# Kernel optimization log

Hardware: AMD Instinct MI355X
Metric: run time of the kernel (lower is better)

The kernel has to match this reference:

```python
import jax, jax.numpy as jnp
import numpy as np

K = 3  # kernel_size

def _bn(x, g, b, m, v, eps=1e-5):
    # inference-mode BatchNorm2d over channel axis 1
    sh = (1, -1, 1, 1)
    return (x - m.reshape(sh)) * (g.reshape(sh) / jnp.sqrt(v.reshape(sh) + eps)) + b.reshape(sh)

def setup_inputs() -> dict:
    key = jax.random.key(0)
    ks = jax.random.split(key, 12)
    B, C, H, W, OC = 8, 128, 96, 96, 256
    k2 = K * K
    x = jax.random.normal(ks[0], (B, C, H, W), jnp.float32)
    # get_weight grouped 1x1 conv: [C*9,1,1,1] stored compactly as [C,9]
    w1 = jax.random.normal(ks[1], (C, k2), jnp.float32) * 0.1
    # generate_feature grouped 3x3 conv (groups=C, multiplier 9): OIHW [C*9,1,3,3]
    gf_w = jax.random.normal(ks[2], (C * k2, 1, K, K), jnp.float32) * 0.1
    bn1_g = jax.random.uniform(ks[3], (C * k2,), jnp.float32, 0.5, 1.5)
    bn1_b = jax.random.normal(ks[4], (C * k2,), jnp.float32) * 0.1
    bn1_m = jax.random.normal(ks[5], (C * k2,), jnp.float32) * 0.1
    bn1_v = jax.random.uniform(ks[6], (C * k2,), jnp.float32, 0.5, 1.5)
    conv_w = jax.random.normal(ks[7], (OC, C, K, K), jnp.float32) * (1.0 / np.sqrt(C * k2))
    conv_b = jax.random.normal(ks[8], (OC,), jnp.float32) * 0.1
    bn2_g = jax.random.uniform(ks[9], (OC,), jnp.float32, 0.5, 1.5)
    bn2_b = jax.random.normal(ks[10], (OC,), jnp.float32) * 0.1
    bn2_m = jax.random.normal(ks[11], (OC,), jnp.float32) * 0.1
    bn2_v = jax.random.uniform(jax.random.fold_in(key, 99), (OC,), jnp.float32, 0.5, 1.5)
    return {"x": x, "w1": w1, "gf_w": gf_w, "bn1_g": bn1_g, "bn1_b": bn1_b,
            "bn1_m": bn1_m, "bn1_v": bn1_v, "conv_w": conv_w, "conv_b": conv_b,
            "bn2_g": bn2_g, "bn2_b": bn2_b, "bn2_m": bn2_m, "bn2_v": bn2_v}

def reference(x, w1, gf_w, bn1_g, bn1_b, bn1_m, bn1_v, conv_w, conv_b, bn2_g, bn2_b, bn2_m, bn2_v):
    B, C, H, W = x.shape
    k2 = K * K
    # --- get_weight: AvgPool2d(k=3, pad=1, stride=1, count_include_pad) + grouped 1x1 conv ---
    pooled = jax.lax.reduce_window(x, 0.0, jax.lax.add, (1, 1, K, K), (1, 1, 1, 1),
                                   [(0, 0), (0, 0), (1, 1), (1, 1)]) / float(k2)
    weight = jnp.einsum('bchw,cn->bcnhw', pooled, w1)  # [B,C,9,H,W]
    attn = jax.nn.softmax(weight, axis=2)
    # --- generate_feature: depthwise 3x3 conv (groups=C, mult 9) + BN + ReLU ---
    feat = jax.lax.conv_general_dilated(x, gf_w, (1, 1), [(1, 1), (1, 1)],
                                        dimension_numbers=('NCHW', 'OIHW', 'NCHW'),
                                        feature_group_count=C)
    feat = jax.nn.relu(_bn(feat, bn1_g, bn1_b, bn1_m, bn1_v)).reshape(B, C, k2, H, W)
    # --- attention reweight + space-to-depth rearrange 'b c (n1 n2) h w -> b c (h n1) (w n2)' ---
    wd = (feat * attn).reshape(B, C, K, K, H, W)
    wd = wd.transpose(0, 1, 4, 2, 5, 3).reshape(B, C, H * K, W * K)
    # --- final conv k=3 stride=3 + BN + ReLU ---
    out = jax.lax.conv_general_dilated(wd, conv_w, (K, K), [(0, 0), (0, 0)],
                                       dimension_numbers=('NCHW', 'OIHW', 'NCHW'))
    out = out + conv_b.reshape(1, -1, 1, 1)
    return jax.nn.relu(_bn(out, bn2_g, bn2_b, bn2_m, bn2_v))
```

## Files before the change

kernel.cpp:

```cpp
#include <hip/hip_runtime.h>
#include <hip/hip_bf16.h>


#define CCH  128
#define OCN  256
#define HH   96
#define WWD  96
#define KCH  1152
#define PIMG 9216
#define BNP  64
#define NBLK 144
#define CC   32
#define KC   288
#define VP   296
#define NT   512

using short8   = __attribute__((ext_vector_type(8))) short;
using f32x4    = __attribute__((ext_vector_type(4))) float;
using f32x2    = __attribute__((ext_vector_type(2))) float;
using ushort2v = __attribute__((ext_vector_type(2))) ushort;

__device__ __forceinline__ ushort bf16bits(float f) {
    __hip_bfloat16 h = __float2bfloat16(f);
    return *reinterpret_cast<ushort*>(&h);
}

struct NB { f32x2 p[4]; float s; };

__global__ void prep_kernel(const float* __restrict__ W2, const float* __restrict__ gfw,
                            const float* __restrict__ bn1g, const float* __restrict__ bn1b,
                            const float* __restrict__ bn1m, const float* __restrict__ bn1v,
                            const float* __restrict__ w1,
                            ushort* __restrict__ W2bf, float* __restrict__ gws,
                            float* __restrict__ shiftv, float* __restrict__ w1s) {
    int i = blockIdx.x * 256 + threadIdx.x;
    if (i < OCN * KCH) {
        W2bf[i] = bf16bits(W2[i]);
    } else if (i < OCN * KCH + KCH) {
        const int ch = i - OCN * KCH;
        const float sc = bn1g[ch] * rsqrtf(bn1v[ch] + 1e-5f);
        shiftv[ch] = bn1b[ch] - bn1m[ch] * sc;
        #pragma unroll
        for (int t = 0; t < 9; ++t) gws[ch * 12 + t] = gfw[ch * 9 + t] * sc;
    } else if (i < OCN * KCH + KCH + CCH) {
        const int c = i - OCN * KCH - KCH;
        #pragma unroll
        for (int n = 0; n < 9; ++n)
            w1s[c * 12 + n] = w1[c * 9 + n] * (1.f / 9.f) * 1.4426950408889634f;
    }
}

template<bool FAST>
__global__ __launch_bounds__(NT, 4) void rfa_dp_kernel(
    const float* __restrict__ x,
    const float* __restrict__ w1,   const float* __restrict__ gfw,
    const float* __restrict__ bn1g, const float* __restrict__ bn1b,
    const float* __restrict__ bn1m, const float* __restrict__ bn1v,
    const float* __restrict__ W2f,
    const ushort* __restrict__ W2bf, const float* __restrict__ gws,
    const float* __restrict__ shiftv, const float* __restrict__ w1s,
    const float* __restrict__ cbias,
    const float* __restrict__ bn2g, const float* __restrict__ bn2b,
    const float* __restrict__ bn2m, const float* __restrict__ bn2v,
    float* __restrict__ out)
{
    __shared__ ushort vlds[2][BNP * VP];

    const int bid = blockIdx.x;
    const int wk  = (bid & 7) * NBLK + (bid >> 3);
    const int b   = wk / NBLK;
    const int P0  = (wk % NBLK) * BNP;

    const int tid  = threadIdx.x;
    const int lane = tid & 63;
    const int wid  = __builtin_amdgcn_readfirstlane(tid >> 6);

    const int px = lane;
    const int p  = P0 + px;
    const int h  = p / WWD;
    const int w  = p - h * WWD;
    const int l15 = lane & 15;
    const int lhi = lane >> 4;

    int off9[9];
    f32x2 okp[4];
    float ok8;
    {
        float okr[3], okc[3];
        int hro[3], wxc[3];
        #pragma unroll
        for (int d = 0; d < 3; ++d) {
            int hy = h + d - 1;
            okr[d] = ((unsigned)hy < (unsigned)HH) ? 1.f : 0.f;
            hro[d] = ((hy < 0) ? 0 : (hy > 95 ? 95 : hy)) * WWD;
            int wx = w + d - 1;
            okc[d] = ((unsigned)wx < (unsigned)WWD) ? 1.f : 0.f;
            wxc[d] = (wx < 0) ? 0 : (wx > 95 ? 95 : wx);
        }
        #pragma unroll
        for (int dy = 0; dy < 3; ++dy)
            #pragma unroll
            for (int dx = 0; dx < 3; ++dx) off9[dy*3+dx] = hro[dy] + wxc[dx];
        okp[0] = f32x2{okr[0]*okc[0], okr[0]*okc[1]};
        okp[1] = f32x2{okr[0]*okc[2], okr[1]*okc[0]};
        okp[2] = f32x2{okr[1]*okc[1], okr[1]*okc[2]};
        okp[3] = f32x2{okr[2]*okc[0], okr[2]*okc[1]};
        ok8    = okr[2]*okc[2];
    }

    f32x4 acc[2][4] = {};
    const float* xb = x + (size_t)b * CCH * PIMG;
    const int abase = (wid * 32 + l15) * KCH + lhi * 8;

    auto chan = [&](int q) { return (q >> 2) * CC + wid * 4 + (q & 3); };
    auto load_nb = [&](int c) {
        const float* xc = xb + (size_t)c * PIMG;
        NB r;
        float v0 = xc[off9[0]], v1 = xc[off9[1]], v2 = xc[off9[2]];
        float v3 = xc[off9[3]], v4 = xc[off9[4]], v5 = xc[off9[5]];
        float v6 = xc[off9[6]], v7 = xc[off9[7]], v8 = xc[off9[8]];
        r.p[0] = f32x2{v0,v1}; r.p[1] = f32x2{v2,v3};
        r.p[2] = f32x2{v4,v5}; r.p[3] = f32x2{v6,v7};
        r.s = v8;
        return r;
    };

    auto produce_one = [&](const NB& nb, int c, int cl, ushort* vbuf, bool evenp) {
        f32x2 e[4];
        #pragma unroll
        for (int i = 0; i < 4; ++i) e[i] = nb.p[i] * okp[i];
        const float e8 = nb.s * ok8;
        f32x2 ps2 = (e[0] + e[1]) + (e[2] + e[3]);
        const float psum = ps2[0] + ps2[1] + e8;

        float at[9], ss = 0.f;
        if constexpr (FAST) {
            const float* w1r = w1s + c * 12;
            #pragma unroll
            for (int n = 0; n < 9; ++n) { at[n] = __builtin_exp2f(psum * w1r[n]); ss += at[n]; }
        } else {
            const float pooled = psum * (1.f / 9.f);
            const float* w1r = w1 + c * 9;
            #pragma unroll
            for (int n = 0; n < 9; ++n) { at[n] = __expf(pooled * w1r[n]); ss += at[n]; }
        }
        const float rs = __builtin_amdgcn_rcpf(ss);

        ushort u[9];
        #pragma unroll
        for (int n = 0; n < 9; ++n) {
            const int ch = c * 9 + n;
            float f;
            if constexpr (FAST) {
                const f32x2* gp = reinterpret_cast<const f32x2*>(gws + ch * 12);
                f32x2 f2 = f32x2{shiftv[ch], 0.f};
                #pragma unroll
                for (int u4 = 0; u4 < 4; ++u4) f2 = __builtin_elementwise_fma(e[u4], gp[u4], f2);
                f = f2[0] + f2[1];
                f = fmaf(e8, gws[ch * 12 + 8], f);
            } else {
                const float* gr = gfw + ch * 9;
                float cv = 0.f;
                cv = fmaf(e[0][0], gr[0], cv); cv = fmaf(e[0][1], gr[1], cv);
                cv = fmaf(e[1][0], gr[2], cv); cv = fmaf(e[1][1], gr[3], cv);
                cv = fmaf(e[2][0], gr[4], cv); cv = fmaf(e[2][1], gr[5], cv);
                cv = fmaf(e[3][0], gr[6], cv); cv = fmaf(e[3][1], gr[7], cv);
                cv = fmaf(e8, gr[8], cv);
                const float sc = bn1g[ch] * rsqrtf(bn1v[ch] + 1e-5f);
                f = (cv - bn1m[ch]) * sc + bn1b[ch];
            }
            f = fmaxf(f, 0.f) * (at[n] * rs);
            u[n] = bf16bits(f);
        }
        ushort* vp = vbuf + px * VP + cl * 9;
        if (evenp) {
            ushort2v* q2 = reinterpret_cast<ushort2v*>(vp);
            q2[0] = ushort2v{u[0], u[1]}; q2[1] = ushort2v{u[2], u[3]};
            q2[2] = ushort2v{u[4], u[5]}; q2[3] = ushort2v{u[6], u[7]};
            vp[8] = u[8];
        } else {
            vp[0] = u[0];
            ushort2v* q2 = reinterpret_cast<ushort2v*>(vp + 1);
            q2[0] = ushort2v{u[1], u[2]}; q2[1] = ushort2v{u[3], u[4]};
            q2[2] = ushort2v{u[5], u[6]}; q2[3] = ushort2v{u[7], u[8]};
        }
    };

    NB arr[4];
    #pragma unroll
    for (int i = 0; i < 4; ++i) arr[i] = load_nb(chan(i));

    for (int ck = 0; ck < 4; ++ck) {
        ushort* vbuf = vlds[ck & 1];

        #pragma unroll
        for (int pp = 0; pp < 4; ++pp) {
            const int q = ck * 4 + pp;
            produce_one(arr[pp], chan(q), wid * 4 + pp, vbuf, (pp & 1) == 0);
            const int qn = (q + 4 > 15) ? 15 : q + 4;
            arr[pp] = load_nb(chan(qn));
        }
        __syncthreads();

        const int k0 = ck * KC;
        #pragma unroll 3
        for (int kk = 0; kk < 9; ++kk) {
            short8 afr[2], bfr[4];
            #pragma unroll
            for (int mi = 0; mi < 2; ++mi) {
                const int ai = abase + mi * 16 * KCH + k0 + kk * 32;
                if constexpr (FAST) {
                    afr[mi] = *reinterpret_cast<const short8*>(W2bf + ai);
                } else {
                    const f32x4 f0 = *reinterpret_cast<const f32x4*>(W2f + ai);
                    const f32x4 f1 = *reinterpret_cast<const f32x4*>(W2f + ai + 4);
                    short8 a;
                    a[0]=(short)bf16bits(f0[0]); a[1]=(short)bf16bits(f0[1]);
                    a[2]=(short)bf16bits(f0[2]); a[3]=(short)bf16bits(f0[3]);
                    a[4]=(short)bf16bits(f1[0]); a[5]=(short)bf16bits(f1[1]);
                    a[6]=(short)bf16bits(f1[2]); a[7]=(short)bf16bits(f1[3]);
                    afr[mi] = a;
                }
            }
            #pragma unroll
            for (int ni = 0; ni < 4; ++ni)
                bfr[ni] = *reinterpret_cast<const short8*>(
                    vbuf + (ni * 16 + l15) * VP + kk * 32 + lhi * 8);
            #pragma unroll
            for (int mi = 0; mi < 2; ++mi)
                #pragma unroll
                for (int ni = 0; ni < 4; ++ni)
                    acc[mi][ni] = __builtin_amdgcn_mfma_f32_16x16x32_bf16(
                        afr[mi], bfr[ni], acc[mi][ni], 0, 0, 0);
        }
    }

    #pragma unroll
    for (int mi = 0; mi < 2; ++mi) {
        #pragma unroll
        for (int r = 0; r < 4; ++r) {
            const int oc = wid * 32 + mi * 16 + lhi * 4 + r;
            const float s2 = bn2g[oc] * rsqrtf(bn2v[oc] + 1e-5f);
            const float t2 = (cbias[oc] - bn2m[oc]) * s2 + bn2b[oc];
            float* op = out + ((size_t)(b * OCN + oc)) * PIMG + P0;
            #pragma unroll
            for (int ni = 0; ni < 4; ++ni)
                op[ni * 16 + l15] = fmaxf(fmaf(acc[mi][ni][r], s2, t2), 0.f);
        }
    }
}

extern "C" void kernel_launch(void* const* d_in, const int* in_sizes, int n_in,
                              void* d_out, int out_size, void* d_ws, size_t ws_size,
                              hipStream_t stream) {
    const float* xx   = (const float*)d_in[0];
    const float* w1   = (const float*)d_in[1];
    const float* gfw  = (const float*)d_in[2];
    const float* bn1g = (const float*)d_in[3];
    const float* bn1b = (const float*)d_in[4];
    const float* bn1m = (const float*)d_in[5];
    const float* bn1v = (const float*)d_in[6];
    const float* W2   = (const float*)d_in[7];
    const float* cb   = (const float*)d_in[8];
    const float* bn2g = (const float*)d_in[9];
    const float* bn2b = (const float*)d_in[10];
    const float* bn2m = (const float*)d_in[11];
    const float* bn2v = (const float*)d_in[12];
    float* o = (float*)d_out;

    const size_t off_gws   = (size_t)OCN * KCH * sizeof(ushort);
    const size_t off_shift = off_gws + (size_t)KCH * 12 * sizeof(float);
    const size_t off_w1s   = off_shift + (size_t)KCH * sizeof(float);
    const size_t ws_need   = off_w1s + (size_t)CCH * 12 * sizeof(float);

    dim3 grid(8 * NBLK);
    dim3 blk(NT);

    if (ws_size >= ws_need) {
        ushort* W2bf = (ushort*)d_ws;
        float*  gwsp = (float*)((char*)d_ws + off_gws);
        float*  shf  = (float*)((char*)d_ws + off_shift);
        float*  w1sp = (float*)((char*)d_ws + off_w1s);
        const int ptot = OCN * KCH + KCH + CCH;
        prep_kernel<<<(ptot + 255) / 256, 256, 0, stream>>>(
            W2, gfw, bn1g, bn1b, bn1m, bn1v, w1, W2bf, gwsp, shf, w1sp);
        rfa_dp_kernel<true><<<grid, blk, 0, stream>>>(
            xx, w1, gfw, bn1g, bn1b, bn1m, bn1v, W2, W2bf, gwsp, shf, w1sp,
            cb, bn2g, bn2b, bn2m, bn2v, o);
    } else {
        rfa_dp_kernel<false><<<grid, blk, 0, stream>>>(
            xx, w1, gfw, bn1g, bn1b, bn1m, bn1v, W2, nullptr, nullptr, nullptr, nullptr,
            cb, bn2g, bn2b, bn2m, bn2v, o);
    }
}
```

Baseline: 228.5 us.

## Use 16 waves per block, each owning 16 output channels and 2 input channels

Doubles the block to 1024 threads so each wave computes a 16-row output channel tile instead of 32, and produces 2 input channels per chunk instead of 4. Register use for accumulators and prefetched neighbourhoods shrinks, and launch bounds request higher occupancy. The intent is to hide the latency of the gather and MFMA phases with more waves. In exchange, each wave loads the shared B fragments for half as many MFMAs, raising LDS read traffic per FLOP, and the loads are software-pipelined only one channel ahead.

```diff
diff --git a/kernel.cpp b/kernel.cpp
--- a/kernel.cpp
+++ b/kernel.cpp
@@ -13,7 +13,7 @@
 #define CC   32
 #define KC   288
 #define VP   296
-#define NT   512
+#define NT   1024
 
 using short8   = __attribute__((ext_vector_type(8))) short;
 using f32x4    = __attribute__((ext_vector_type(4))) float;
@@ -51,7 +51,7 @@
 }
 
 template<bool FAST>
-__global__ __launch_bounds__(NT, 4) void rfa_dp_kernel(
+__global__ __launch_bounds__(NT, 8) void rfa_w16_kernel(
     const float* __restrict__ x,
     const float* __restrict__ w1,   const float* __restrict__ gfw,
     const float* __restrict__ bn1g, const float* __restrict__ bn1b,
@@ -108,11 +108,11 @@
         ok8    = okr[2]*okc[2];
     }
 
-    f32x4 acc[2][4] = {};
+    f32x4 acc[4] = {};
     const float* xb = x + (size_t)b * CCH * PIMG;
-    const int abase = (wid * 32 + l15) * KCH + lhi * 8;
-
-    auto chan = [&](int q) { return (q >> 2) * CC + wid * 4 + (q & 3); };
+    const int abase = (wid * 16 + l15) * KCH + lhi * 8;
+
+    auto chan = [&](int q) { return (q >> 1) * CC + wid * 2 + (q & 1); };
     auto load_nb = [&](int c) {
         const float* xc = xb + (size_t)c * PIMG;
         NB r;
@@ -186,67 +186,59 @@
         }
     };
 
-    NB arr[4];
-    #pragma unroll
-    for (int i = 0; i < 4; ++i) arr[i] = load_nb(chan(i));
+    NB nb = load_nb(chan(0));
 
     for (int ck = 0; ck < 4; ++ck) {
         ushort* vbuf = vlds[ck & 1];
 
         #pragma unroll
-        for (int pp = 0; pp < 4; ++pp) {
-            const int q = ck * 4 + pp;
-            produce_one(arr[pp], chan(q), wid * 4 + pp, vbuf, (pp & 1) == 0);
-            const int qn = (q + 4 > 15) ? 15 : q + 4;
-            arr[pp] = load_nb(chan(qn));
+        for (int t = 0; t < 2; ++t) {
+            const int q  = ck * 2 + t;
+            const int qn = (q + 1 > 7) ? 7 : q + 1;
+            NB nbn = load_nb(chan(qn));
+            const int cl = wid * 2 + t;
+            produce_one(nb, chan(q), cl, vbuf, t == 0);
+            nb = nbn;
         }
         __syncthreads();
 
         const int k0 = ck * KC;
         #pragma unroll 3
         for (int kk = 0; kk < 9; ++kk) {
-            short8 afr[2], bfr[4];
-            #pragma unroll
-            for (int mi = 0; mi < 2; ++mi) {
-                const int ai = abase + mi * 16 * KCH + k0 + kk * 32;
-                if constexpr (FAST) {
-                    afr[mi] = *reinterpret_cast<const short8*>(W2bf + ai);
-                } else {
-                    const f32x4 f0 = *reinterpret_cast<const f32x4*>(W2f + ai);
-                    const f32x4 f1 = *reinterpret_cast<const f32x4*>(W2f + ai + 4);
-                    short8 a;
-                    a[0]=(short)bf16bits(f0[0]); a[1]=(short)bf16bits(f0[1]);
-                    a[2]=(short)bf16bits(f0[2]); a[3]=(short)bf16bits(f0[3]);
-                    a[4]=(short)bf16bits(f1[0]); a[5]=(short)bf16bits(f1[1]);
-                    a[6]=(short)bf16bits(f1[2]); a[7]=(short)bf16bits(f1[3]);
-                    afr[mi] = a;
-                }
+            short8 afr, bfr[4];
+            const int ai = abase + k0 + kk * 32;
+            if constexpr (FAST) {
+                afr = *reinterpret_cast<const short8*>(W2bf + ai);
+            } else {
+                const f32x4 f0 = *reinterpret_cast<const f32x4*>(W2f + ai);
+                const f32x4 f1 = *reinterpret_cast<const f32x4*>(W2f + ai + 4);
+                short8 a;
+                a[0]=(short)bf16bits(f0[0]); a[1]=(short)bf16bits(f0[1]);
+                a[2]=(short)bf16bits(f0[2]); a[3]=(short)bf16bits(f0[3]);
+                a[4]=(short)bf16bits(f1[0]); a[5]=(short)bf16bits(f1[1]);
+                a[6]=(short)bf16bits(f1[2]); a[7]=(short)bf16bits(f1[3]);
+                afr = a;
             }
             #pragma unroll
             for (int ni = 0; ni < 4; ++ni)
                 bfr[ni] = *reinterpret_cast<const short8*>(
                     vbuf + (ni * 16 + l15) * VP + kk * 32 + lhi * 8);
             #pragma unroll
-            for (int mi = 0; mi < 2; ++mi)
-                #pragma unroll
-                for (int ni = 0; ni < 4; ++ni)
-                    acc[mi][ni] = __builtin_amdgcn_mfma_f32_16x16x32_bf16(
-                        afr[mi], bfr[ni], acc[mi][ni], 0, 0, 0);
+            for (int ni = 0; ni < 4; ++ni)
+                acc[ni] = __builtin_amdgcn_mfma_f32_16x16x32_bf16(
+                    afr, bfr[ni], acc[ni], 0, 0, 0);
         }
     }
 
     #pragma unroll
-    for (int mi = 0; mi < 2; ++mi) {
-        #pragma unroll
-        for (int r = 0; r < 4; ++r) {
-            const int oc = wid * 32 + mi * 16 + lhi * 4 + r;
-            const float s2 = bn2g[oc] * rsqrtf(bn2v[oc] + 1e-5f);
-            const float t2 = (cbias[oc] - bn2m[oc]) * s2 + bn2b[oc];
-            float* op = out + ((size_t)(b * OCN + oc)) * PIMG + P0;
-            #pragma unroll
-            for (int ni = 0; ni < 4; ++ni)
-                op[ni * 16 + l15] = fmaxf(fmaf(acc[mi][ni][r], s2, t2), 0.f);
-        }
+    for (int r = 0; r < 4; ++r) {
+        const int oc = wid * 16 + lhi * 4 + r;
+        const float s2 = bn2g[oc] * rsqrtf(bn2v[oc] + 1e-5f);
+        const float t2 = (cbias[oc] - bn2m[oc]) * s2 + bn2b[oc];
+        float* op = out + ((size_t)(b * OCN + oc)) * PIMG + P0;
+        #pragma unroll
+        for (int ni = 0; ni < 4; ++ni)
+            op[ni * 16 + l15] = fmaxf(fmaf(acc[ni][r], s2, t2), 0.f);
     }
 }
 
@@ -284,11 +276,11 @@
         const int ptot = OCN * KCH + KCH + CCH;
         prep_kernel<<<(ptot + 255) / 256, 256, 0, stream>>>(
             W2, gfw, bn1g, bn1b, bn1m, bn1v, w1, W2bf, gwsp, shf, w1sp);
-        rfa_dp_kernel<true><<<grid, blk, 0, stream>>>(
+        rfa_w16_kernel<true><<<grid, blk, 0, stream>>>(
             xx, w1, gfw, bn1g, bn1b, bn1m, bn1v, W2, W2bf, gwsp, shf, w1sp,
             cb, bn2g, bn2b, bn2m, bn2v, o);
     } else {
-        rfa_dp_kernel<false><<<grid, blk, 0, stream>>>(
+        rfa_w16_kernel<false><<<grid, blk, 0, stream>>>(
             xx, w1, gfw, bn1g, bn1b, bn1m, bn1v, W2, nullptr, nullptr, nullptr, nullptr,
             cb, bn2g, bn2b, bn2m, bn2v, o);
     }
```

After: 294.1 us. 28.7% more time.

## Split fused producer/GEMM into separate feature-production and MFMA GEMM kernels

Applied to the files above, without the earlier changes.

When the workspace is large enough, the fused kernel is split in two. A producer kernel computes the attention-weighted feature matrix in bf16 and writes it to global memory (about 170 MB). A separate GEMM kernel then streams that matrix through double-buffered LDS tiles into MFMA. The aim is to decouple the VALU-heavy producer from the matrix phase and let each kernel run at higher occupancy, at the cost of a large extra global write plus re-read. The fallback fused kernel is also restructured to prefetch one channel at a time and store elements individually.

```diff
diff --git a/kernel.cpp b/kernel.cpp
--- a/kernel.cpp
+++ b/kernel.cpp
@@ -10,10 +10,12 @@
 #define PIMG 9216
 #define BNP  64
 #define NBLK 144
+#define NT   512
 #define CC   32
 #define KC   288
 #define VP   296
-#define NT   512
+#define KCB  192
+#define VPB  200
 
 using short8   = __attribute__((ext_vector_type(8))) short;
 using f32x4    = __attribute__((ext_vector_type(4))) float;
@@ -50,8 +52,217 @@
     }
 }
 
+__global__ __launch_bounds__(NT, 8) void rfa_prod_kernel(
+    const float* __restrict__ x,
+    const float* __restrict__ gws, const float* __restrict__ shiftv,
+    const float* __restrict__ w1s,
+    ushort* __restrict__ vout)
+{
+    __shared__ ushort tile[BNP * VP];
+
+    const int bid = blockIdx.x;
+    const int wk  = (bid & 7) * NBLK + (bid >> 3);
+    const int b   = wk / NBLK;
+    const int P0  = (wk % NBLK) * BNP;
+
+    const int tid  = threadIdx.x;
+    const int lane = tid & 63;
+    const int wid  = __builtin_amdgcn_readfirstlane(tid >> 6);
+
+    const int px = lane;
+    const int p  = P0 + px;
+    const int h  = p / WWD;
+    const int w  = p - h * WWD;
+
+    int off9[9];
+    f32x2 okp[4];
+    float ok8;
+    {
+        float okr[3], okc[3];
+        int hro[3], wxc[3];
+        #pragma unroll
+        for (int d = 0; d < 3; ++d) {
+            int hy = h + d - 1;
+            okr[d] = ((unsigned)hy < (unsigned)HH) ? 1.f : 0.f;
+            hro[d] = ((hy < 0) ? 0 : (hy > 95 ? 95 : hy)) * WWD;
+            int wx = w + d - 1;
+            okc[d] = ((unsigned)wx < (unsigned)WWD) ? 1.f : 0.f;
+            wxc[d] = (wx < 0) ? 0 : (wx > 95 ? 95 : wx);
+        }
+        #pragma unroll
+        for (int dy = 0; dy < 3; ++dy)
+            #pragma unroll
+            for (int dx = 0; dx < 3; ++dx) off9[dy*3+dx] = hro[dy] + wxc[dx];
+        okp[0] = f32x2{okr[0]*okc[0], okr[0]*okc[1]};
+        okp[1] = f32x2{okr[0]*okc[2], okr[1]*okc[0]};
+        okp[2] = f32x2{okr[1]*okc[1], okr[1]*okc[2]};
+        okp[3] = f32x2{okr[2]*okc[0], okr[2]*okc[1]};
+        ok8    = okr[2]*okc[2];
+    }
+
+    const float* xb = x + (size_t)b * CCH * PIMG;
+    auto chan = [&](int q) { return (q >> 2) * CC + wid * 4 + (q & 3); };
+    auto load_nb = [&](int c) {
+        const float* xc = xb + (size_t)c * PIMG;
+        NB r;
+        float v0 = xc[off9[0]], v1 = xc[off9[1]], v2 = xc[off9[2]];
+        float v3 = xc[off9[3]], v4 = xc[off9[4]], v5 = xc[off9[5]];
+        float v6 = xc[off9[6]], v7 = xc[off9[7]], v8 = xc[off9[8]];
+        r.p[0] = f32x2{v0,v1}; r.p[1] = f32x2{v2,v3};
+        r.p[2] = f32x2{v4,v5}; r.p[3] = f32x2{v6,v7};
+        r.s = v8;
+        return r;
+    };
+
+    auto produce_one = [&](const NB& nb, int c, int cl, bool evenp) {
+        f32x2 e[4];
+        #pragma unroll
+        for (int i = 0; i < 4; ++i) e[i] = nb.p[i] * okp[i];
+        const float e8 = nb.s * ok8;
+        f32x2 ps2 = (e[0] + e[1]) + (e[2] + e[3]);
+        const float psum = ps2[0] + ps2[1] + e8;
+
+        float at[9], ss = 0.f;
+        const float* w1r = w1s + c * 12;
+        #pragma unroll
+        for (int n = 0; n < 9; ++n) { at[n] = __builtin_exp2f(psum * w1r[n]); ss += at[n]; }
+        const float rs = __builtin_amdgcn_rcpf(ss);
+
+        ushort u[9];
+        #pragma unroll
+        for (int n = 0; n < 9; ++n) {
+            const int ch = c * 9 + n;
+            const f32x2* gp = reinterpret_cast<const f32x2*>(gws + ch * 12);
+            f32x2 f2 = f32x2{shiftv[ch], 0.f};
+            #pragma unroll
+            for (int u4 = 0; u4 < 4; ++u4) f2 = __builtin_elementwise_fma(e[u4], gp[u4], f2);
+            float f = f2[0] + f2[1];
+            f = fmaf(e8, gws[ch * 12 + 8], f);
+            f = fmaxf(f, 0.f) * (at[n] * rs);
+            u[n] = bf16bits(f);
+        }
+        ushort* vp = tile + px * VP + cl * 9;
+        if (evenp) {
+            ushort2v* q2 = reinterpret_cast<ushort2v*>(vp);
+            q2[0] = ushort2v{u[0], u[1]}; q2[1] = ushort2v{u[2], u[3]};
+            q2[2] = ushort2v{u[4], u[5]}; q2[3] = ushort2v{u[6], u[7]};
+            vp[8] = u[8];
+        } else {
+            vp[0] = u[0];
+            ushort2v* q2 = reinterpret_cast<ushort2v*>(vp + 1);
+            q2[0] = ushort2v{u[1], u[2]}; q2[1] = ushort2v{u[3], u[4]};
+            q2[2] = ushort2v{u[5], u[6]}; q2[3] = ushort2v{u[7], u[8]};
+        }
+    };
+
+    NB nb = load_nb(chan(0));
+    for (int ck = 0; ck < 4; ++ck) {
+        #pragma unroll
+        for (int t = 0; t < 4; ++t) {
+            const int q  = ck * 4 + t;
+            const int qn = (q + 1 > 15) ? 15 : q + 1;
+            NB nbn = load_nb(chan(qn));
+            produce_one(nb, chan(q), wid * 4 + t, (t & 1) == 0);
+            nb = nbn;
+        }
+        __syncthreads();
+
+        const uint* lw = reinterpret_cast<const uint*>(tile);
+        uint* vd = reinterpret_cast<uint*>(vout);
+        #pragma unroll
+        for (int i = 0; i < 18; ++i) {
+            const int flat = i * 512 + tid;
+            const int row  = flat / 144;
+            const int col  = flat - row * 144;
+            vd[(size_t)(b * PIMG + P0 + row) * 576 + ck * 144 + col] = lw[row * 148 + col];
+        }
+        __syncthreads();
+    }
+}
+
+__global__ __launch_bounds__(NT, 4) void rfa_gemm_kernel(
+    const ushort* __restrict__ W2bf, const ushort* __restrict__ v,
+    const float* __restrict__ cbias,
+    const float* __restrict__ bn2g, const float* __restrict__ bn2b,
+    const float* __restrict__ bn2m, const float* __restrict__ bn2v,
+    float* __restrict__ out)
+{
+    __shared__ ushort vt[2][BNP * VPB];
+
+    const int bid = blockIdx.x;
+    const int wk  = (bid & 7) * NBLK + (bid >> 3);
+    const int b   = wk / NBLK;
+    const int P0  = (wk % NBLK) * BNP;
+
+    const int tid  = threadIdx.x;
+    const int lane = tid & 63;
+    const int wid  = __builtin_amdgcn_readfirstlane(tid >> 6);
+    const int l15  = lane & 15;
+    const int lhi  = lane >> 4;
+
+    const ushort* vrow = v + (size_t)(b * PIMG + P0) * KCH;
+    const int abase = (wid * 32 + l15) * KCH + lhi * 8;
+
+    f32x4 acc[2][4] = {};
+
+    auto stage = [&](int ck, ushort* buf) {
+        #pragma unroll
+        for (int u = 0; u < 3; ++u) {
+            const int flat = u * 512 + tid;
+            const int row  = flat / 24;
+            const int col  = flat - row * 24;
+            const short8 val = *reinterpret_cast<const short8*>(
+                vrow + (size_t)row * KCH + ck * KCB + col * 8);
+            *reinterpret_cast<short8*>(buf + row * VPB + col * 8) = val;
+        }
+    };
+    auto gemm = [&](int ck, const ushort* buf) {
+        const int k0 = ck * KCB;
+        #pragma unroll
+        for (int kk = 0; kk < 6; ++kk) {
+            short8 afr[2], bfr[4];
+            #pragma unroll
+            for (int mi = 0; mi < 2; ++mi)
+                afr[mi] = *reinterpret_cast<const short8*>(
+                    W2bf + abase + mi * 16 * KCH + k0 + kk * 32);
+            #pragma unroll
+            for (int ni = 0; ni < 4; ++ni)
+                bfr[ni] = *reinterpret_cast<const short8*>(
+                    buf + (ni * 16 + l15) * VPB + kk * 32 + lhi * 8);
+            #pragma unroll
+            for (int mi = 0; mi < 2; ++mi)
+                #pragma unroll
+                for (int ni = 0; ni < 4; ++ni)
+                    acc[mi][ni] = __builtin_amdgcn_mfma_f32_16x16x32_bf16(
+                        afr[mi], bfr[ni], acc[mi][ni], 0, 0, 0);
+        }
+    };
+
+    stage(0, vt[0]);
+    __syncthreads();
+    for (int ck = 0; ck < 6; ++ck) {
+        if (ck < 5) stage(ck + 1, vt[(ck + 1) & 1]);
+        gemm(ck, vt[ck & 1]);
+        __syncthreads();
+    }
+
+    #pragma unroll
+    for (int mi = 0; mi < 2; ++mi) {
+        #pragma unroll
+        for (int r = 0; r < 4; ++r) {
+            const int oc = wid * 32 + mi * 16 + lhi * 4 + r;
+            const float s2 = bn2g[oc] * rsqrtf(bn2v[oc] + 1e-5f);
+            const float t2 = (cbias[oc] - bn2m[oc]) * s2 + bn2b[oc];
+            float* op = out + ((size_t)(b * OCN + oc)) * PIMG + P0;
+            #pragma unroll
+            for (int ni = 0; ni < 4; ++ni)
+                op[ni * 16 + l15] = fmaxf(fmaf(acc[mi][ni][r], s2, t2), 0.f);
+        }
+    }
+}
+
 template<bool FAST>
-__global__ __launch_bounds__(NT, 4) void rfa_dp_kernel(
+__global__ __launch_bounds__(NT, 4) void rfa_mfma3_kernel(
     const float* __restrict__ x,
     const float* __restrict__ w1,   const float* __restrict__ gfw,
     const float* __restrict__ bn1g, const float* __restrict__ bn1b,
@@ -66,28 +277,23 @@
 {
     __shared__ ushort vlds[2][BNP * VP];
 
-    const int bid = blockIdx.x;
-    const int wk  = (bid & 7) * NBLK + (bid >> 3);
-    const int b   = wk / NBLK;
-    const int P0  = (wk % NBLK) * BNP;
-
-    const int tid  = threadIdx.x;
-    const int lane = tid & 63;
-    const int wid  = __builtin_amdgcn_readfirstlane(tid >> 6);
-
-    const int px = lane;
-    const int p  = P0 + px;
-    const int h  = p / WWD;
-    const int w  = p - h * WWD;
-    const int l15 = lane & 15;
-    const int lhi = lane >> 4;
-
-    int off9[9];
+    const int tid = threadIdx.x;
+    const int b   = blockIdx.x / NBLK;
+    const int P0  = (blockIdx.x % NBLK) * BNP;
+
+    const int px  = tid & 63;
+    const int p   = P0 + px;
+    const int h   = p / WWD;
+    const int w   = p - h * WWD;
+    const int wid = __builtin_amdgcn_readfirstlane(tid >> 6);
+    const int l15 = px & 15;
+    const int lhi = px >> 4;
+
+    int hro[3], wxc[3];
     f32x2 okp[4];
     float ok8;
     {
         float okr[3], okc[3];
-        int hro[3], wxc[3];
         #pragma unroll
         for (int d = 0; d < 3; ++d) {
             int hy = h + d - 1;
@@ -97,10 +303,6 @@
             okc[d] = ((unsigned)wx < (unsigned)WWD) ? 1.f : 0.f;
             wxc[d] = (wx < 0) ? 0 : (wx > 95 ? 95 : wx);
         }
-        #pragma unroll
-        for (int dy = 0; dy < 3; ++dy)
-            #pragma unroll
-            for (int dx = 0; dx < 3; ++dx) off9[dy*3+dx] = hro[dy] + wxc[dx];
         okp[0] = f32x2{okr[0]*okc[0], okr[0]*okc[1]};
         okp[1] = f32x2{okr[0]*okc[2], okr[1]*okc[0]};
         okp[2] = f32x2{okr[1]*okc[1], okr[1]*okc[2]};
@@ -113,92 +315,77 @@
     const int abase = (wid * 32 + l15) * KCH + lhi * 8;
 
     auto chan = [&](int q) { return (q >> 2) * CC + wid * 4 + (q & 3); };
-    auto load_nb = [&](int c) {
+    auto load_nb2 = [&](int c) {
         const float* xc = xb + (size_t)c * PIMG;
         NB r;
-        float v0 = xc[off9[0]], v1 = xc[off9[1]], v2 = xc[off9[2]];
-        float v3 = xc[off9[3]], v4 = xc[off9[4]], v5 = xc[off9[5]];
-        float v6 = xc[off9[6]], v7 = xc[off9[7]], v8 = xc[off9[8]];
+        float v0 = xc[hro[0]+wxc[0]], v1 = xc[hro[0]+wxc[1]], v2 = xc[hro[0]+wxc[2]];
+        float v3 = xc[hro[1]+wxc[0]], v4 = xc[hro[1]+wxc[1]], v5 = xc[hro[1]+wxc[2]];
+        float v6 = xc[hro[2]+wxc[0]], v7 = xc[hro[2]+wxc[1]], v8 = xc[hro[2]+wxc[2]];
         r.p[0] = f32x2{v0,v1}; r.p[1] = f32x2{v2,v3};
         r.p[2] = f32x2{v4,v5}; r.p[3] = f32x2{v6,v7};
         r.s = v8;
         return r;
     };
 
-    auto produce_one = [&](const NB& nb, int c, int cl, ushort* vbuf, bool evenp) {
-        f32x2 e[4];
-        #pragma unroll
-        for (int i = 0; i < 4; ++i) e[i] = nb.p[i] * okp[i];
-        const float e8 = nb.s * ok8;
-        f32x2 ps2 = (e[0] + e[1]) + (e[2] + e[3]);
-        const float psum = ps2[0] + ps2[1] + e8;
-
-        float at[9], ss = 0.f;
-        if constexpr (FAST) {
-            const float* w1r = w1s + c * 12;
-            #pragma unroll
-            for (int n = 0; n < 9; ++n) { at[n] = __builtin_exp2f(psum * w1r[n]); ss += at[n]; }
-        } else {
-            const float pooled = psum * (1.f / 9.f);
-            const float* w1r = w1 + c * 9;
-            #pragma unroll
-            for (int n = 0; n < 9; ++n) { at[n] = __expf(pooled * w1r[n]); ss += at[n]; }
-        }
-        const float rs = __builtin_amdgcn_rcpf(ss);
-
-        ushort u[9];
-        #pragma unroll
-        for (int n = 0; n < 9; ++n) {
-            const int ch = c * 9 + n;
-            float f;
-            if constexpr (FAST) {
-                const f32x2* gp = reinterpret_cast<const f32x2*>(gws + ch * 12);
-                f32x2 f2 = f32x2{shiftv[ch], 0.f};
-                #pragma unroll
-                for (int u4 = 0; u4 < 4; ++u4) f2 = __builtin_elementwise_fma(e[u4], gp[u4], f2);
-                f = f2[0] + f2[1];
-                f = fmaf(e8, gws[ch * 12 + 8], f);
-            } else {
-                const float* gr = gfw + ch * 9;
-                float cv = 0.f;
-                cv = fmaf(e[0][0], gr[0], cv); cv = fmaf(e[0][1], gr[1], cv);
-                cv = fmaf(e[1][0], gr[2], cv); cv = fmaf(e[1][1], gr[3], cv);
-                cv = fmaf(e[2][0], gr[4], cv); cv = fmaf(e[2][1], gr[5], cv);
-                cv = fmaf(e[3][0], gr[6], cv); cv = fmaf(e[3][1], gr[7], cv);
-                cv = fmaf(e8, gr[8], cv);
-                const float sc = bn1g[ch] * rsqrtf(bn1v[ch] + 1e-5f);
-                f = (cv - bn1m[ch]) * sc + bn1b[ch];
-            }
-            f = fmaxf(f, 0.f) * (at[n] * rs);
-            u[n] = bf16bits(f);
-        }
-        ushort* vp = vbuf + px * VP + cl * 9;
-        if (evenp) {
-            ushort2v* q2 = reinterpret_cast<ushort2v*>(vp);
-            q2[0] = ushort2v{u[0], u[1]}; q2[1] = ushort2v{u[2], u[3]};
-            q2[2] = ushort2v{u[4], u[5]}; q2[3] = ushort2v{u[6], u[7]};
-            vp[8] = u[8];
-        } else {
-            vp[0] = u[0];
-            ushort2v* q2 = reinterpret_cast<ushort2v*>(vp + 1);
-            q2[0] = ushort2v{u[1], u[2]}; q2[1] = ushort2v{u[3], u[4]};
-            q2[2] = ushort2v{u[5], u[6]}; q2[3] = ushort2v{u[7], u[8]};
-        }
-    };
-
-    NB arr[4];
-    #pragma unroll
-    for (int i = 0; i < 4; ++i) arr[i] = load_nb(chan(i));
+    NB nb = load_nb2(chan(0));
 
     for (int ck = 0; ck < 4; ++ck) {
         ushort* vbuf = vlds[ck & 1];
-
-        #pragma unroll
-        for (int pp = 0; pp < 4; ++pp) {
-            const int q = ck * 4 + pp;
-            produce_one(arr[pp], chan(q), wid * 4 + pp, vbuf, (pp & 1) == 0);
-            const int qn = (q + 4 > 15) ? 15 : q + 4;
-            arr[pp] = load_nb(chan(qn));
+        #pragma unroll
+        for (int pass = 0; pass < 4; ++pass) {
+            const int q  = ck * 4 + pass;
+            const int qn = (q + 1 > 15) ? 15 : q + 1;
+            NB nbn = load_nb2(chan(qn));
+
+            const int c  = chan(q);
+            const int cl = wid * 4 + pass;
+            f32x2 e[4];
+            #pragma unroll
+            for (int i = 0; i < 4; ++i) e[i] = nb.p[i] * okp[i];
+            const float e8 = nb.s * ok8;
+            f32x2 ps2 = (e[0] + e[1]) + (e[2] + e[3]);
+            const float psum = ps2[0] + ps2[1] + e8;
+
+            float at[9], ss = 0.f;
+            if constexpr (FAST) {
+                const float* w1r = w1s + c * 12;
+                #pragma unroll
+                for (int n = 0; n < 9; ++n) { at[n] = __builtin_exp2f(psum * w1r[n]); ss += at[n]; }
+            } else {
+                const float pooled = psum * (1.f / 9.f);
+                const float* w1r = w1 + c * 9;
+                #pragma unroll
+                for (int n = 0; n < 9; ++n) { at[n] = __expf(pooled * w1r[n]); ss += at[n]; }
+            }
+            const float rs = __builtin_amdgcn_rcpf(ss);
+
+            ushort* vp = vbuf + px * VP + cl * 9;
+            #pragma unroll
+            for (int n = 0; n < 9; ++n) {
+                const int ch = c * 9 + n;
+                float f;
+                if constexpr (FAST) {
+                    const f32x2* gp = reinterpret_cast<const f32x2*>(gws + ch * 12);
+                    f32x2 f2 = f32x2{shiftv[ch], 0.f};
+                    #pragma unroll
+                    for (int u4 = 0; u4 < 4; ++u4) f2 = __builtin_elementwise_fma(e[u4], gp[u4], f2);
+                    f = f2[0] + f2[1];
+                    f = fmaf(e8, gws[ch * 12 + 8], f);
+                } else {
+                    const float* gr = gfw + ch * 9;
+                    float cv = 0.f;
+                    cv = fmaf(e[0][0], gr[0], cv); cv = fmaf(e[0][1], gr[1], cv);
+                    cv = fmaf(e[1][0], gr[2], cv); cv = fmaf(e[1][1], gr[3], cv);
+                    cv = fmaf(e[2][0], gr[4], cv); cv = fmaf(e[2][1], gr[5], cv);
+                    cv = fmaf(e[3][0], gr[6], cv); cv = fmaf(e[3][1], gr[7], cv);
+                    cv = fmaf(e8, gr[8], cv);
+                    const float sc = bn1g[ch] * rsqrtf(bn1v[ch] + 1e-5f);
+                    f = (cv - bn1m[ch]) * sc + bn1b[ch];
+                }
+                f = fmaxf(f, 0.f) * (at[n] * rs);
+                vp[n] = bf16bits(f);
+            }
+            nb = nbn;
         }
         __syncthreads();
 
@@ -268,27 +455,42 @@
     const float* bn2v = (const float*)d_in[12];
     float* o = (float*)d_out;
 
-    const size_t off_gws   = (size_t)OCN * KCH * sizeof(ushort);
-    const size_t off_shift = off_gws + (size_t)KCH * 12 * sizeof(float);
-    const size_t off_w1s   = off_shift + (size_t)KCH * sizeof(float);
-    const size_t ws_need   = off_w1s + (size_t)CCH * 12 * sizeof(float);
-
+    const size_t v_bytes   = (size_t)8 * PIMG * KCH * sizeof(ushort);
+    const size_t w2_bytes  = (size_t)OCN * KCH * sizeof(ushort);
+    const size_t gws_bytes = (size_t)KCH * 12 * sizeof(float);
+    const size_t shf_bytes = (size_t)KCH * sizeof(float);
+    const size_t w1s_bytes = (size_t)CCH * 12 * sizeof(float);
+
+    const size_t split_need = v_bytes + w2_bytes + gws_bytes + shf_bytes + w1s_bytes;
+    const size_t fused_need = w2_bytes + gws_bytes + shf_bytes + w1s_bytes;
+
+    const int ptot = OCN * KCH + KCH + CCH;
     dim3 grid(8 * NBLK);
     dim3 blk(NT);
 
-    if (ws_size >= ws_need) {
-        ushort* W2bf = (ushort*)d_ws;
-        float*  gwsp = (float*)((char*)d_ws + off_gws);
-        float*  shf  = (float*)((char*)d_ws + off_shift);
-        float*  w1sp = (float*)((char*)d_ws + off_w1s);
-        const int ptot = OCN * KCH + KCH + CCH;
+    if (ws_size >= split_need) {
+        ushort* vbuf = (ushort*)d_ws;
+        ushort* W2bf = (ushort*)((char*)d_ws + v_bytes);
+        float*  gwsp = (float*)((char*)d_ws + v_bytes + w2_bytes);
+        float*  shf  = (float*)((char*)gwsp + gws_bytes);
+        float*  w1sp = (float*)((char*)shf + shf_bytes);
         prep_kernel<<<(ptot + 255) / 256, 256, 0, stream>>>(
             W2, gfw, bn1g, bn1b, bn1m, bn1v, w1, W2bf, gwsp, shf, w1sp);
-        rfa_dp_kernel<true><<<grid, blk, 0, stream>>>(
+        rfa_prod_kernel<<<grid, blk, 0, stream>>>(xx, gwsp, shf, w1sp, vbuf);
+        rfa_gemm_kernel<<<grid, blk, 0, stream>>>(
+            W2bf, vbuf, cb, bn2g, bn2b, bn2m, bn2v, o);
+    } else if (ws_size >= fused_need) {
+        ushort* W2bf = (ushort*)d_ws;
+        float*  gwsp = (float*)((char*)d_ws + w2_bytes);
+        float*  shf  = (float*)((char*)gwsp + gws_bytes);
+        float*  w1sp = (float*)((char*)shf + shf_bytes);
+        prep_kernel<<<(ptot + 255) / 256, 256, 0, stream>>>(
+            W2, gfw, bn1g, bn1b, bn1m, bn1v, w1, W2bf, gwsp, shf, w1sp);
+        rfa_mfma3_kernel<true><<<grid, blk, 0, stream>>>(
             xx, w1, gfw, bn1g, bn1b, bn1m, bn1v, W2, W2bf, gwsp, shf, w1sp,
             cb, bn2g, bn2b, bn2m, bn2v, o);
     } else {
-        rfa_dp_kernel<false><<<grid, blk, 0, stream>>>(
+        rfa_mfma3_kernel<false><<<grid, blk, 0, stream>>>(
             xx, w1, gfw, bn1g, bn1b, bn1m, bn1v, W2, nullptr, nullptr, nullptr, nullptr,
             cb, bn2g, bn2b, bn2m, bn2v, o);
     }
```

Result: slower. 446.0 us (+95.2%).
